# Kernel optimization log

Measured on AMD Instinct MI355X. Metric: run time of the kernel, lower is better.

## Reference

```python
import jax, jax.numpy as jnp
import numpy as np

P = 1  # padding (= kernel_size // 2 for 3x3 convs), matches init_kwargs


def _rot(a, k):
    # torch x.rot90(k, dims=(-2, -1)) equivalent
    return jnp.rot90(a, k, axes=(-2, -1))


def _tl(p, top, lft):
    # interpolated top-left corner for equatorial faces (no shared pixel)
    ret = jnp.zeros(top.shape[:-2] + (p, p), top.dtype)
    ret = ret.at[..., -1, -1].set(0.5 * top[..., -1, 0] + 0.5 * lft[..., 0, -1])
    for i in range(1, p):
        ret = ret.at[..., -i - 1, -i:].set(top[..., -i - 1, :i])
        ret = ret.at[..., -i:, -i - 1].set(lft[..., :i, -i - 1])
        ret = ret.at[..., -i - 1, -i - 1].set(0.5 * top[..., -i - 1, 0] + 0.5 * lft[..., 0, -i - 1])
    return ret


def _br(p, b, r):
    # interpolated bottom-right corner for equatorial faces
    ret = jnp.zeros(b.shape[:-2] + (p, p), b.dtype)
    ret = ret.at[..., 0, 0].set(0.5 * b[..., 0, -1] + 0.5 * r[..., -1, 0])
    for i in range(1, p):
        ret = ret.at[..., :i, i].set(r[..., -i:, i])
        ret = ret.at[..., i, :i].set(b[..., i, -i:])
        ret = ret.at[..., i, i].set(0.5 * b[..., i, -1] + 0.5 * r[..., -1, i])
    return ret


def _pn(p, c, t, tl, lft, bl, b, br, rgt, tr):
    # north polar face: top neighbour rotated +90deg, top-left +180deg
    c = jnp.concatenate([_rot(t, 1)[..., -p:, :], c, b[..., :p, :]], axis=-2)
    left = jnp.concatenate([_rot(tl, 2)[..., -p:, -p:], _rot(lft, -1)[..., -p:], bl[..., :p, -p:]], axis=-2)
    right = jnp.concatenate([tr[..., -p:, :p], rgt[..., :p], br[..., :p, :p]], axis=-2)
    return jnp.concatenate([left, c, right], axis=-1)


def _pe(p, c, t, tl, lft, bl, b, br, rgt, tr):
    # equatorial face: no rotations
    c = jnp.concatenate([t[..., -p:, :], c, b[..., :p, :]], axis=-2)
    left = jnp.concatenate([tl[..., -p:, -p:], lft[..., -p:], bl[..., :p, -p:]], axis=-2)
    right = jnp.concatenate([tr[..., -p:, :p], rgt[..., :p], br[..., :p, :p]], axis=-2)
    return jnp.concatenate([left, c, right], axis=-1)


def _ps(p, c, t, tl, lft, bl, b, br, rgt, tr):
    # south polar face: bottom +90deg, right -90deg, bottom-right +180deg
    c = jnp.concatenate([t[..., -p:, :], c, _rot(b, 1)[..., :p, :]], axis=-2)
    left = jnp.concatenate([tl[..., -p:, -p:], lft[..., -p:], bl[..., :p, -p:]], axis=-2)
    right = jnp.concatenate([tr[..., -p:, :p], _rot(rgt, -1)[..., :p], _rot(br, 2)[..., :p, :p]], axis=-2)
    return jnp.concatenate([left, c, right], axis=-1)


def _healpix_pad(x, p):
    B12, C, n, _ = x.shape
    x5 = x.reshape(B12 // 12, 12, C, n, n)  # (B, 12, C, n, n)
    f = [x5[:, i] for i in range(12)]
    pads = [
        _pn(p, f[0], f[1], f[2], f[3], f[3], f[4], f[8], f[5], f[1]),
        _pn(p, f[1], f[2], f[3], f[0], f[0], f[5], f[9], f[6], f[2]),
        _pn(p, f[2], f[3], f[0], f[1], f[1], f[6], f[10], f[7], f[3]),
        _pn(p, f[3], f[0], f[1], f[2], f[2], f[7], f[11], f[4], f[0]),
        _pe(p, f[4], f[0], _tl(p, f[0], f[3]), f[3], f[7], f[11], _br(p, f[11], f[8]), f[8], f[5]),
        _pe(p, f[5], f[1], _tl(p, f[1], f[0]), f[0], f[4], f[8], _br(p, f[8], f[9]), f[9], f[6]),
        _pe(p, f[6], f[2], _tl(p, f[2], f[1]), f[1], f[5], f[9], _br(p, f[9], f[10]), f[10], f[7]),
        _pe(p, f[7], f[3], _tl(p, f[3], f[2]), f[2], f[6], f[10], _br(p, f[10], f[11]), f[11], f[4]),
        _ps(p, f[8], f[5], f[0], f[4], f[11], f[11], f[10], f[9], f[9]),
        _ps(p, f[9], f[6], f[1], f[5], f[8], f[8], f[11], f[10], f[10]),
        _ps(p, f[10], f[7], f[2], f[6], f[9], f[9], f[8], f[11], f[11]),
        _ps(p, f[11], f[4], f[3], f[7], f[10], f[10], f[9], f[8], f[8]),
    ]
    out = jnp.stack(pads, axis=1)  # (B, 12, C, n+2p, n+2p)
    return out.reshape(B12, C, n + 2 * p, n + 2 * p)


def setup_inputs() -> dict:
    key = jax.random.key(0)
    x = jax.random.normal(key, (24, 128, 128, 128), dtype=jnp.float32)
    return {"x": x}


def reference(x):
    return _healpix_pad(x, P)
```

## Files before the change

kernel.cpp:

```cpp
#include <hip/hip_runtime.h>


#define NPLANE_OUT 16900
#define QUADS 4225

__device__ __forceinline__ float hp_face(const float* __restrict__ in, size_t baseoff,
                                         int q, int i, int j) {
  return in[baseoff + ((size_t)q << 21) + (i << 7) + j];
}

__device__ __forceinline__ float hp_val(const float* __restrict__ in, size_t baseoff,
                                        int type, int m, int face, int r, int col) {
  if ((unsigned)(r - 1) < 128u && (unsigned)(col - 1) < 128u)
    return hp_face(in, baseoff, face, r - 1, col - 1);

  const int L = 127;
  if (r == 0) {
    if (col == 0) {
      if (type == 0) return hp_face(in, baseoff, (m + 2) & 3, 0, 0);
      if (type == 1) return 0.5f * (hp_face(in, baseoff, m, L, 0) +
                                    hp_face(in, baseoff, (m + 3) & 3, 0, L));
      return hp_face(in, baseoff, m, L, L);
    }
    if (col == 129) {
      if (type == 0) return hp_face(in, baseoff, (m + 1) & 3, L, 0);
      if (type == 1) return hp_face(in, baseoff, 4 + ((m + 1) & 3), L, 0);
      return hp_face(in, baseoff, 8 + ((m + 1) & 3), L, 0);
    }
    int j = col - 1;
    if (type == 0) return hp_face(in, baseoff, (m + 1) & 3, j, 0);
    if (type == 1) return hp_face(in, baseoff, m, L, j);
    return hp_face(in, baseoff, 4 + ((m + 1) & 3), L, j);
  }
  if (r == 129) {
    if (col == 0) {
      if (type == 0) return hp_face(in, baseoff, (m + 3) & 3, 0, L);
      if (type == 1) return hp_face(in, baseoff, 4 + ((m + 3) & 3), 0, L);
      return hp_face(in, baseoff, 8 + ((m + 3) & 3), 0, L);
    }
    if (col == 129) {
      if (type == 0) return hp_face(in, baseoff, 8 + m, 0, 0);
      if (type == 1) return 0.5f * (hp_face(in, baseoff, 8 + ((m + 3) & 3), 0, L) +
                                    hp_face(in, baseoff, 8 + m, L, 0));
      return hp_face(in, baseoff, 8 + ((m + 2) & 3), L, L);
    }
    int j = col - 1;
    if (type == 0) return hp_face(in, baseoff, 4 + m, 0, j);
    if (type == 1) return hp_face(in, baseoff, 8 + ((m + 3) & 3), 0, j);
    return hp_face(in, baseoff, 8 + ((m + 3) & 3), j, L);
  }
  int i = r - 1;
  if (col == 0) {
    if (type == 0) return hp_face(in, baseoff, (m + 3) & 3, 0, i);
    if (type == 1) return hp_face(in, baseoff, (m + 3) & 3, i, L);
    return hp_face(in, baseoff, 4 + m, i, L);
  }
  if (type == 0) return hp_face(in, baseoff, 4 + ((m + 1) & 3), i, 0);
  if (type == 1) return hp_face(in, baseoff, 8 + m, i, 0);
  return hp_face(in, baseoff, 8 + ((m + 1) & 3), L, i);
}

__global__ __launch_bounds__(256) void CREDITHEALPix_90975997264316_kernel(
    const float* __restrict__ in, float* __restrict__ out) {
  int q = blockIdx.x * 256 + threadIdx.x;
  if (q >= QUADS) return;
  int plane = blockIdx.y;
  int b12 = plane >> 7;
  int c = plane & 127;
  int batch = (b12 >= 12) ? 1 : 0;
  int face = b12 - batch * 12;
  int type = face >> 2;
  int m = face & 3;
  size_t baseoff = (((size_t)batch * 12 * 128) + (size_t)c) << 14;

  int flat0 = q * 4;
  unsigned r0 = (unsigned)flat0 / 130u;
  unsigned c0 = (unsigned)flat0 - r0 * 130u;

  float4 v;
  if (r0 >= 1u && r0 <= 128u && c0 >= 1u && c0 <= 125u) {
    const float* src = in + baseoff + ((size_t)face << 21) +
                       ((size_t)(r0 - 1) << 7) + (c0 - 1);
    v.x = src[0]; v.y = src[1]; v.z = src[2]; v.w = src[3];
  } else {
    float tmp[4];
#pragma unroll
    for (int k = 0; k < 4; ++k) {
      int flat = flat0 + k;
      unsigned r = (unsigned)flat / 130u;
      unsigned col = (unsigned)flat - r * 130u;
      tmp[k] = hp_val(in, baseoff, type, m, face, (int)r, (int)col);
    }
    v.x = tmp[0]; v.y = tmp[1]; v.z = tmp[2]; v.w = tmp[3];
  }
  *(float4*)(out + (size_t)plane * NPLANE_OUT + flat0) = v;
}

extern "C" void kernel_launch(void* const* d_in, const int* in_sizes, int n_in,
                              void* d_out, int out_size, void* d_ws, size_t ws_size,
                              hipStream_t stream) {
  const float* in = (const float*)d_in[0];
  float* out = (float*)d_out;
  dim3 grid(17, 3072, 1);
  dim3 block(256, 1, 1);
  CREDITHEALPix_90975997264316_kernel<<<grid, block, 0, stream>>>(in, out);
}
```

Measured before the change: 367.1 us.

## Split interior and halo work: aligned vector loads for interior, separate border block

The work is split by block: 16 blocks per plane copy the 128x128 interior using aligned 16-byte input loads, and one extra block per plane writes the 516 halo elements. The old version iterated over output quads, which gave misaligned scalar input loads and sent border quads down a branchy path. Input reads are now aligned, but output stores are misaligned because rows are 130 wide, and the border block does little work.

Result: no change. 361.4 us (-1.5%).

```diff
diff --git a/kernel.cpp b/kernel.cpp
--- a/kernel.cpp
+++ b/kernel.cpp
@@ -2,7 +2,6 @@
 
 
 #define NPLANE_OUT 16900
-#define QUADS 4225
 
 __device__ __forceinline__ float hp_face(const float* __restrict__ in, size_t baseoff,
                                          int q, int i, int j) {
@@ -11,9 +10,6 @@
 
 __device__ __forceinline__ float hp_val(const float* __restrict__ in, size_t baseoff,
                                         int type, int m, int face, int r, int col) {
-  if ((unsigned)(r - 1) < 128u && (unsigned)(col - 1) < 128u)
-    return hp_face(in, baseoff, face, r - 1, col - 1);
-
   const int L = 127;
   if (r == 0) {
     if (col == 0) {
@@ -60,10 +56,10 @@
   return hp_face(in, baseoff, 8 + ((m + 1) & 3), L, i);
 }
 
+typedef float f4v __attribute__((ext_vector_type(4)));
+
 __global__ __launch_bounds__(256) void CREDITHEALPix_90975997264316_kernel(
     const float* __restrict__ in, float* __restrict__ out) {
-  int q = blockIdx.x * 256 + threadIdx.x;
-  if (q >= QUADS) return;
   int plane = blockIdx.y;
   int b12 = plane >> 7;
   int c = plane & 127;
@@ -71,29 +67,26 @@
   int face = b12 - batch * 12;
   int type = face >> 2;
   int m = face & 3;
-  size_t baseoff = (((size_t)batch * 12 * 128) + (size_t)c) << 14;
+  size_t baseoff = (((size_t)batch * 1536) + (size_t)c) << 14;
+  size_t face_off = baseoff + ((size_t)face << 21);
+  float* __restrict__ oplane = out + (size_t)plane * NPLANE_OUT;
 
-  int flat0 = q * 4;
-  unsigned r0 = (unsigned)flat0 / 130u;
-  unsigned c0 = (unsigned)flat0 - r0 * 130u;
-
-  float4 v;
-  if (r0 >= 1u && r0 <= 128u && c0 >= 1u && c0 <= 125u) {
-    const float* src = in + baseoff + ((size_t)face << 21) +
-                       ((size_t)(r0 - 1) << 7) + (c0 - 1);
-    v.x = src[0]; v.y = src[1]; v.z = src[2]; v.w = src[3];
+  if (blockIdx.x < 16) {
+    int iq = blockIdx.x * 256 + threadIdx.x;
+    int r = iq >> 5;
+    int j4 = (iq & 31) << 2;
+    f4v v = *(const f4v*)(in + face_off + ((size_t)r << 7) + j4);
+    __builtin_memcpy(oplane + (r + 1) * 130 + 1 + j4, &v, 16);
   } else {
-    float tmp[4];
-#pragma unroll
-    for (int k = 0; k < 4; ++k) {
-      int flat = flat0 + k;
-      unsigned r = (unsigned)flat / 130u;
-      unsigned col = (unsigned)flat - r * 130u;
-      tmp[k] = hp_val(in, baseoff, type, m, face, (int)r, (int)col);
+    for (int e = threadIdx.x; e < 516; e += 256) {
+      int r, col;
+      if (e < 130)      { r = 0;       col = e; }
+      else if (e < 260) { r = 129;     col = e - 130; }
+      else if (e < 388) { r = e - 259; col = 0; }
+      else              { r = e - 387; col = 129; }
+      oplane[r * 130 + col] = hp_val(in, baseoff, type, m, face, r, col);
     }
-    v.x = tmp[0]; v.y = tmp[1]; v.z = tmp[2]; v.w = tmp[3];
   }
-  *(float4*)(out + (size_t)plane * NPLANE_OUT + flat0) = v;
 }
 
 extern "C" void kernel_launch(void* const* d_in, const int* in_sizes, int n_in,
```
